# Kernel tuning notes

Hardware: AMD Instinct MI355X
Metric: run time of the kernel (lower is better)

## Reference

```python
import jax, jax.numpy as jnp
import numpy as np

EMBED = 1024
HEADS = 16
HEAD_DIM = EMBED // HEADS
B, S = 4, 2048


def setup_inputs() -> dict:
    key = jax.random.key(0)
    ks = jax.random.split(key, 12)
    scale = 1.0 / np.sqrt(EMBED)
    inp = {
        'query': jax.random.normal(ks[0], (B, S, EMBED), jnp.float32),
        'key_in': jax.random.normal(ks[1], (B, S, EMBED), jnp.float32),
        'value': jax.random.normal(ks[2], (B, S, EMBED), jnp.float32),
        'mask': jnp.tril(jnp.ones((S, S), jnp.int32))[None, None],  # causal [1,1,S,S]
        'Wq': jax.random.normal(ks[3], (EMBED, EMBED), jnp.float32) * scale,
        'bq': jnp.zeros((EMBED,), jnp.float32),
        'Wk': jax.random.normal(ks[4], (EMBED, EMBED), jnp.float32) * scale,
        'bk': jnp.zeros((EMBED,), jnp.float32),
        'Wv': jax.random.normal(ks[5], (EMBED, EMBED), jnp.float32) * scale,
        'bv': jnp.zeros((EMBED,), jnp.float32),
        'Wo': jax.random.normal(ks[6], (EMBED, EMBED), jnp.float32) * scale,
        'bo': jnp.zeros((EMBED,), jnp.float32),
    }
    return inp


def reference(query, key_in, value, mask, Wq, bq, Wk, bk, Wv, bv, Wo, bo):
    b = query.shape[0]
    # projections (torch Linear: x @ W.T + b)
    Q = query @ Wq.T + bq
    K = key_in @ Wk.T + bk
    V = value @ Wv.T + bv
    # [B, H, S, Dh]
    Q = Q.reshape(b, -1, HEADS, HEAD_DIM).transpose(0, 2, 1, 3)
    K = K.reshape(b, -1, HEADS, HEAD_DIM).transpose(0, 2, 1, 3)
    V = V.reshape(b, -1, HEADS, HEAD_DIM).transpose(0, 2, 1, 3)
    scores = jnp.einsum('bhqd,bhkd->bhqk', Q, K) / np.sqrt(HEAD_DIM)
    scores = jnp.where(mask == 0, jnp.float32(-1e20), scores)
    probs = jax.nn.softmax(scores, axis=-1)  # dropout p=0 (eval)
    attn = jnp.einsum('bhqk,bhkd->bhqd', probs, V)
    attn = attn.transpose(0, 2, 1, 3).reshape(b, -1, EMBED)
    return attn @ Wo.T + bo
```

## Files before the change

### kernel.cpp

```cpp
#include <hip/hip_runtime.h>
#include <type_traits>

typedef unsigned short u16;
typedef __bf16 bf16x8 __attribute__((ext_vector_type(8)));
typedef float f32x4 __attribute__((ext_vector_type(4)));

#define EMBED   1024
#define HEADS   16
#define HEAD_DIM 64
#define BATCH   4
#define SEQ     2048
#define MROWS   (BATCH * SEQ)

__device__ __forceinline__ u16 f2bf(float f) {
  union { __bf16 h; u16 u; } c;
  c.h = (__bf16)f;
  return c.u;
}

__device__ __forceinline__ bf16x8 cvt8(const float* p) {
  const float4 a = *(const float4*)p;
  const float4 b = *(const float4*)(p + 4);
  bf16x8 r;
  r[0] = (__bf16)a.x; r[1] = (__bf16)a.y; r[2] = (__bf16)a.z; r[3] = (__bf16)a.w;
  r[4] = (__bf16)b.x; r[5] = (__bf16)b.y; r[6] = (__bf16)b.z; r[7] = (__bf16)b.w;
  return r;
}

__device__ __forceinline__ void gload16(const u16* g, u16* lds) {
  __builtin_amdgcn_global_load_lds(
      (const __attribute__((address_space(1))) void*)g,
      (__attribute__((address_space(3))) void*)lds, 16, 0, 0);
}

__global__ __launch_bounds__(256) void cvt_bf16(
    const float* __restrict__ src, u16* __restrict__ dst, int n8)
{
  const int i = blockIdx.x * 256 + threadIdx.x;
  if (i < n8) *(bf16x8*)(dst + (size_t)i * 8) = cvt8(src + (size_t)i * 8);
}

__global__ __launch_bounds__(256) void cvt_fused(
    const float* q,  u16* dq,
    const float* k,  u16* dk,
    const float* wq, u16* dwq,
    const float* wk, u16* dwk,
    const float* wv, u16* dwv,
    const float* wo, u16* dwo,
    int n8t, int n8w)
{
  int i = blockIdx.x * 256 + threadIdx.x;
  if (i < n8t) { *(bf16x8*)(dq + (size_t)i * 8) = cvt8(q + (size_t)i * 8); return; }
  i -= n8t;
  if (i < n8t) { *(bf16x8*)(dk + (size_t)i * 8) = cvt8(k + (size_t)i * 8); return; }
  i -= n8t;
  if (i < n8w) { *(bf16x8*)(dwq + (size_t)i * 8) = cvt8(wq + (size_t)i * 8); return; }
  i -= n8w;
  if (i < n8w) { *(bf16x8*)(dwk + (size_t)i * 8) = cvt8(wk + (size_t)i * 8); return; }
  i -= n8w;
  if (i < n8w) { *(bf16x8*)(dwv + (size_t)i * 8) = cvt8(wv + (size_t)i * 8); return; }
  i -= n8w;
  if (dwo && i < n8w) { *(bf16x8*)(dwo + (size_t)i * 8) = cvt8(wo + (size_t)i * 8); }
}

__device__ __forceinline__ void swz_block(int& m0, int& n0) {
  const int gx = 8;
  int bid = blockIdx.y * gx + blockIdx.x;
  const int cpx = (gx * 64) >> 3;
  bid = (bid & 7) * cpx + (bid >> 3);
  m0 = (bid / gx) * 128;
  n0 = (bid - (bid / gx) * gx) * 128;
}

template<typename TB, typename TC>
__global__ __launch_bounds__(256) void gemm_bt(
    const u16* __restrict__ A, const TB* __restrict__ Bw,
    const float* __restrict__ bias, TC* __restrict__ C,
    int M, int N, int K)
{
  __shared__ __align__(16) u16 As[128][32];
  __shared__ __align__(16) u16 Bs[128][32];
  const int t    = threadIdx.x;
  const int lane = t & 63;
  const int wave = t >> 6;
  const int quad = lane >> 4;
  const int lr   = lane & 15;
  int m0, n0;
  swz_block(m0, n0);
  const int wr = (wave >> 1) * 64;
  const int wc = (wave & 1) * 64;
  const int gr = lane >> 2;
  const int gc = (lane & 3) * 8;

  f32x4 acc[4][4] = {};

  for (int k0 = 0; k0 < K; k0 += 32) {
    gload16(&A[(size_t)(m0 + 16 * wave + gr) * K + k0 + gc],      &As[16 * wave][0]);
    gload16(&A[(size_t)(m0 + 64 + 16 * wave + gr) * K + k0 + gc], &As[64 + 16 * wave][0]);
    if constexpr (std::is_same<TB, u16>::value) {
      gload16(&Bw[(size_t)(n0 + 16 * wave + gr) * K + k0 + gc],      &Bs[16 * wave][0]);
      gload16(&Bw[(size_t)(n0 + 64 + 16 * wave + gr) * K + k0 + gc], &Bs[64 + 16 * wave][0]);
    } else {
      const int srr = t >> 2, src = (t & 3) * 8;
      *(bf16x8*)&Bs[srr][src]      = cvt8(&Bw[(size_t)(n0 + srr) * K + k0 + src]);
      *(bf16x8*)&Bs[64 + srr][src] = cvt8(&Bw[(size_t)(n0 + 64 + srr) * K + k0 + src]);
    }
    __syncthreads();
    bf16x8 af[4], bfr[4];
#pragma unroll
    for (int i = 0; i < 4; ++i) af[i]  = *(const bf16x8*)&As[wr + i * 16 + lr][quad * 8];
#pragma unroll
    for (int i = 0; i < 4; ++i) bfr[i] = *(const bf16x8*)&Bs[wc + i * 16 + lr][quad * 8];
#pragma unroll
    for (int mi = 0; mi < 4; ++mi)
#pragma unroll
      for (int ni = 0; ni < 4; ++ni)
        acc[mi][ni] = __builtin_amdgcn_mfma_f32_16x16x32_bf16(af[mi], bfr[ni], acc[mi][ni], 0, 0, 0);
    __syncthreads();
  }

#pragma unroll
  for (int mi = 0; mi < 4; ++mi)
#pragma unroll
    for (int ni = 0; ni < 4; ++ni) {
      const int col = n0 + wc + ni * 16 + lr;
      const float bv = bias[col];
#pragma unroll
      for (int r = 0; r < 4; ++r) {
        const int row = m0 + wr + mi * 16 + quad * 4 + r;
        const float v = acc[mi][ni][r] + bv;
        if constexpr (std::is_same<TC, u16>::value)
          C[(size_t)row * N + col] = f2bf(v);
        else
          C[(size_t)row * N + col] = v;
      }
    }
}

__global__ __launch_bounds__(256) void gemm_vt(
    const u16* __restrict__ A, const u16* __restrict__ Bw,
    const float* __restrict__ bias, u16* __restrict__ Vt,
    int M, int N, int K)
{
  __shared__ __align__(16) u16 As[128][32];
  __shared__ __align__(16) u16 Bs[128][32];
  const int t    = threadIdx.x;
  const int lane = t & 63;
  const int wave = t >> 6;
  const int quad = lane >> 4;
  const int lr   = lane & 15;
  int m0, n0;
  swz_block(m0, n0);
  const int wr = (wave >> 1) * 64;
  const int wc = (wave & 1) * 64;
  const int gr = lane >> 2;
  const int gc = (lane & 3) * 8;

  f32x4 acc[4][4] = {};

  for (int k0 = 0; k0 < K; k0 += 32) {
    gload16(&A[(size_t)(m0 + 16 * wave + gr) * K + k0 + gc],       &As[16 * wave][0]);
    gload16(&A[(size_t)(m0 + 64 + 16 * wave + gr) * K + k0 + gc],  &As[64 + 16 * wave][0]);
    gload16(&Bw[(size_t)(n0 + 16 * wave + gr) * K + k0 + gc],      &Bs[16 * wave][0]);
    gload16(&Bw[(size_t)(n0 + 64 + 16 * wave + gr) * K + k0 + gc], &Bs[64 + 16 * wave][0]);
    __syncthreads();
    bf16x8 af[4], bfr[4];
#pragma unroll
    for (int i = 0; i < 4; ++i) af[i]  = *(const bf16x8*)&As[wr + i * 16 + lr][quad * 8];
#pragma unroll
    for (int i = 0; i < 4; ++i) bfr[i] = *(const bf16x8*)&Bs[wc + i * 16 + lr][quad * 8];
#pragma unroll
    for (int mi = 0; mi < 4; ++mi)
#pragma unroll
      for (int ni = 0; ni < 4; ++ni)
        acc[mi][ni] = __builtin_amdgcn_mfma_f32_16x16x32_bf16(af[mi], bfr[ni], acc[mi][ni], 0, 0, 0);
    __syncthreads();
  }

#pragma unroll
  for (int mi = 0; mi < 4; ++mi)
#pragma unroll
    for (int ni = 0; ni < 4; ++ni) {
      const int col = n0 + wc + ni * 16 + lr;
      const int hh = col >> 6, dd = col & 63;
      const float bv = bias[col];
      const int row0 = m0 + wr + mi * 16 + quad * 4;
      const int bb = row0 >> 11, s0 = row0 & 2047;
      u16 pk[4];
#pragma unroll
      for (int r = 0; r < 4; ++r) pk[r] = f2bf(acc[mi][ni][r] + bv);
      *(ushort4*)&Vt[((size_t)((bb * 16 + hh) * 64 + dd)) * SEQ + s0] = *(ushort4*)pk;
    }
}

#define QS_OFF 0
#define PS_OFF (64 * 72)
#define KV_OFF (2 * 64 * 72)
#define TILE_SZ (64 * 64)
__global__ __launch_bounds__(256, 3) void flash5(
    const u16* __restrict__ Qbf, const u16* __restrict__ Wqb,
    const float* __restrict__ bq,
    const u16* __restrict__ Kp, const u16* __restrict__ Vt,
    u16* __restrict__ AO)
{
  __shared__ __align__(16) u16 smem[KV_OFF + 4 * TILE_SZ];
  u16 (*Qs)[72] = (u16(*)[72])(smem + QS_OFF);
  u16 (*Ps)[72] = (u16(*)[72])(smem + PS_OFF);

  const int t    = threadIdx.x;
  const int lane = t & 63;
  const int wave = t >> 6;
  const int quad = lane >> 4;
  const int lr   = lane & 15;
  const int bh = blockIdx.x;
  const int pr = blockIdx.y;
  const int b  = bh >> 4, h = bh & 15;
  const size_t rowbase = (size_t)b * SEQ;
  const int hcol = h * HEAD_DIM;
  const int wrow = wave * 16;
  const int sr = lane >> 3;
  const int sc = ((lane & 7) ^ sr) * 8;

  auto frag = [&](int off, int row, int chunk) -> bf16x8 {
    return *(const bf16x8*)(smem + off + row * 64 + ((chunk ^ (row & 7)) << 3));
  };

  int q0 = 0;

  auto stageQW = [&](int bi, int k0) {
    const int ko = KV_OFF + bi * TILE_SZ;
    const int vo = KV_OFF + (2 + bi) * TILE_SZ;
#pragma unroll
    for (int c8 = 0; c8 < 2; ++c8) {
      const int g = wrow + c8 * 8;
      gload16(&Qbf[(rowbase + q0 + g + sr) * EMBED + k0 + sc], smem + ko + g * 64);
      gload16(&Wqb[(size_t)(hcol + g + sr) * EMBED + k0 + sc], smem + vo + g * 64);
    }
  };
  auto stageKV = [&](int bi, int j) {
    const int kb = j * 64;
    const int ko = KV_OFF + bi * TILE_SZ;
    const int vo = KV_OFF + (2 + bi) * TILE_SZ;
#pragma unroll
    for (int c8 = 0; c8 < 2; ++c8) {
      const int g = wrow + c8 * 8;
      gload16(&Kp[(rowbase + kb + g + sr) * EMBED + hcol + sc], smem + ko + g * 64);
      gload16(&Vt[((size_t)bh * 64 + g + sr) * SEQ + kb + sc],  smem + vo + g * 64);
    }
  };

  for (int half = 0; half < 2; ++half) {
    const int qi = half ? (31 - pr) : pr;
    q0 = qi * 64;

    f32x4 qacc[4] = {};
    stageQW(0, 0);
    __syncthreads();
    for (int s = 0; s < 16; ++s) {
      if (s < 15) stageQW((s + 1) & 1, (s + 1) * 64);
      const int ao = KV_OFF + (s & 1) * TILE_SZ;
      const int bo = KV_OFF + (2 + (s & 1)) * TILE_SZ;
#pragma unroll
      for (int ks = 0; ks < 2; ++ks) {
        const bf16x8 aq = frag(ao, wrow + lr, ks * 4 + quad);
        bf16x8 bw[4];
#pragma unroll
        for (int mi = 0; mi < 4; ++mi) bw[mi] = frag(bo, mi * 16 + lr, ks * 4 + quad);
        __builtin_amdgcn_s_setprio(1);
#pragma unroll
        for (int mi = 0; mi < 4; ++mi)
          qacc[mi] = __builtin_amdgcn_mfma_f32_16x16x32_bf16(bw[mi], aq, qacc[mi], 0, 0, 0);
        __builtin_amdgcn_s_setprio(0);
      }
      __syncthreads();
    }
#pragma unroll
    for (int mi = 0; mi < 4; ++mi) {
      const float4 bv4 = *(const float4*)&bq[hcol + mi * 16 + quad * 4];
      union { ushort4 v; u16 e[4]; } pk;
      pk.e[0] = f2bf(qacc[mi][0] + bv4.x);
      pk.e[1] = f2bf(qacc[mi][1] + bv4.y);
      pk.e[2] = f2bf(qacc[mi][2] + bv4.z);
      pk.e[3] = f2bf(qacc[mi][3] + bv4.w);
      *(ushort4*)&Qs[wrow + lr][mi * 16 + quad * 4] = pk.v;
    }

    f32x4 o_acc[4] = {};
    float lsum = 0.f;

    stageKV(0, 0);
    __syncthreads();
    for (int j = 0; j <= qi; ++j) {
      if (j < qi) stageKV((j + 1) & 1, j + 1);
      const int ko = KV_OFF + (j & 1) * TILE_SZ;
      const int vo = KV_OFF + (2 + (j & 1)) * TILE_SZ;

      f32x4 st[4] = {};
#pragma unroll
      for (int ks = 0; ks < 2; ++ks) {
        const bf16x8 a = *(const bf16x8*)&Qs[wrow + lr][ks * 32 + quad * 8];
        bf16x8 bk[4];
#pragma unroll
        for (int mi = 0; mi < 4; ++mi) bk[mi] = frag(ko, mi * 16 + lr, ks * 4 + quad);
        __builtin_amdgcn_s_setprio(1);
#pragma unroll
        for (int mi = 0; mi < 4; ++mi)
          st[mi] = __builtin_amdgcn_mfma_f32_16x16x32_bf16(bk[mi], a, st[mi], 0, 0, 0);
        __builtin_amdgcn_s_setprio(0);
      }
      const bool diag = (j == qi);
#pragma unroll
      for (int mi = 0; mi < 4; ++mi) {
        union { ushort4 v; u16 e[4]; } pk;
#pragma unroll
        for (int r = 0; r < 4; ++r) {
          float p = __expf(st[mi][r] * 0.125f);
          if (diag && (mi * 16 + quad * 4 + r > wrow + lr)) p = 0.f;
          lsum += p;
          pk.e[r] = f2bf(p);
        }
        *(ushort4*)&Ps[wrow + lr][mi * 16 + quad * 4] = pk.v;
      }
#pragma unroll
      for (int ks = 0; ks < 2; ++ks) {
        const bf16x8 ap = *(const bf16x8*)&Ps[wrow + lr][ks * 32 + quad * 8];
        bf16x8 bv[4];
#pragma unroll
        for (int nd = 0; nd < 4; ++nd) bv[nd] = frag(vo, nd * 16 + lr, ks * 4 + quad);
        __builtin_amdgcn_s_setprio(1);
#pragma unroll
        for (int nd = 0; nd < 4; ++nd)
          o_acc[nd] = __builtin_amdgcn_mfma_f32_16x16x32_bf16(ap, bv[nd], o_acc[nd], 0, 0, 0);
        __builtin_amdgcn_s_setprio(0);
      }
      __syncthreads();
    }

    lsum += __shfl_xor(lsum, 16);
    lsum += __shfl_xor(lsum, 32);
    float linv[4];
#pragma unroll
    for (int r = 0; r < 4; ++r)
      linv[r] = 1.0f / __shfl(lsum, quad * 4 + r);
#pragma unroll
    for (int nd = 0; nd < 4; ++nd)
#pragma unroll
      for (int r = 0; r < 4; ++r)
        AO[(rowbase + q0 + wrow + quad * 4 + r) * EMBED + hcol + nd * 16 + lr]
            = f2bf(o_acc[nd][r] * linv[r]);
  }
}

extern "C" void kernel_launch(void* const* d_in, const int* in_sizes, int n_in,
                              void* d_out, int out_size, void* d_ws, size_t ws_size,
                              hipStream_t stream) {
  const float* query  = (const float*)d_in[0];
  const float* key_in = (const float*)d_in[1];
  const float* value  = (const float*)d_in[2];
  const float* Wq = (const float*)d_in[4];
  const float* bq = (const float*)d_in[5];
  const float* Wk = (const float*)d_in[6];
  const float* bk = (const float*)d_in[7];
  const float* Wv = (const float*)d_in[8];
  const float* bv = (const float*)d_in[9];
  const float* Wo = (const float*)d_in[10];
  const float* bo = (const float*)d_in[11];
  float* out = (float*)d_out;

  const size_t tsz = (size_t)MROWS * EMBED;
  const size_t wsz = (size_t)EMBED * EMBED;

  u16* Kp = (u16*)d_ws;
  u16* Vt = Kp + tsz;
  const bool wo_bf = (ws_size >= (2 * tsz + wsz) * sizeof(u16));
  u16* Wob = wo_bf ? (Vt + tsz) : nullptr;

  u16* Qbf = (u16*)d_out;
  u16* Wqb = Qbf + tsz;
  u16* Wkb = Wqb + wsz;
  u16* Wvb = Wkb + wsz;

  u16* Kbf = (u16*)d_in[3];
  u16* Vbf = Kbf;
  u16* AO  = Kbf;

  dim3 blk(256);
  const int n8t = (int)(tsz / 8), n8w = (int)(wsz / 8);

  {
    const int total = 2 * n8t + (wo_bf ? 4 : 3) * n8w;
    cvt_fused<<<(total + 255) / 256, blk, 0, stream>>>(
        query, Qbf, key_in, Kbf, Wq, Wqb, Wk, Wkb, Wv, Wvb, Wo, Wob, n8t, n8w);
  }

  dim3 gproj(EMBED / 128, MROWS / 128);
  gemm_bt<u16, u16><<<gproj, blk, 0, stream>>>(Kbf, Wkb, bk, Kp, MROWS, EMBED, EMBED);

  cvt_bf16<<<n8t / 256, blk, 0, stream>>>(value, Vbf, n8t);
  gemm_vt<<<gproj, blk, 0, stream>>>(Vbf, Wvb, bv, Vt, MROWS, EMBED, EMBED);

  dim3 gattn(BATCH * HEADS, 16);
  flash5<<<gattn, blk, 0, stream>>>(Qbf, Wqb, bq, Kp, Vt, AO);

  if (wo_bf)
    gemm_bt<u16, float><<<gproj, blk, 0, stream>>>(AO, Wob, bo, out, MROWS, EMBED, EMBED);
  else
    gemm_bt<float, float><<<gproj, blk, 0, stream>>>(AO, Wo, bo, out, MROWS, EMBED, EMBED);
}
```

Measured before the change: 365.9 us.

## Fuse fp32 conversion into a batched QKV projection GEMM and simplify attention

Replaces the separate fp32-to-bf16 activation conversion kernels and the separate K and V projection GEMMs with one batched qkv_gemm launch (grid z over Q/K/V). That kernel converts fp32 inputs to bf16 while staging them into LDS. The Q projection moves out of the attention kernel, so flash6 just loads a precomputed Q tile instead of recomputing Q from Wq in every block. This removes extra activation round-trips through memory and several kernel launches. In exchange, the A operand is now loaded synchronously through registers rather than with direct-to-LDS loads, and the Q projection buffer is placed in the output buffer.

```diff
diff --git a/kernel.cpp b/kernel.cpp
--- a/kernel.cpp
+++ b/kernel.cpp
@@ -33,27 +33,12 @@
       (__attribute__((address_space(3))) void*)lds, 16, 0, 0);
 }
 
-__global__ __launch_bounds__(256) void cvt_bf16(
-    const float* __restrict__ src, u16* __restrict__ dst, int n8)
-{
-  const int i = blockIdx.x * 256 + threadIdx.x;
-  if (i < n8) *(bf16x8*)(dst + (size_t)i * 8) = cvt8(src + (size_t)i * 8);
-}
-
-__global__ __launch_bounds__(256) void cvt_fused(
-    const float* q,  u16* dq,
-    const float* k,  u16* dk,
-    const float* wq, u16* dwq,
-    const float* wk, u16* dwk,
-    const float* wv, u16* dwv,
-    const float* wo, u16* dwo,
-    int n8t, int n8w)
+__global__ __launch_bounds__(256) void cvt_w(
+    const float* wq, u16* dwq, const float* wk, u16* dwk,
+    const float* wv, u16* dwv, const float* wo, u16* dwo,
+    int n8w)
 {
   int i = blockIdx.x * 256 + threadIdx.x;
-  if (i < n8t) { *(bf16x8*)(dq + (size_t)i * 8) = cvt8(q + (size_t)i * 8); return; }
-  i -= n8t;
-  if (i < n8t) { *(bf16x8*)(dk + (size_t)i * 8) = cvt8(k + (size_t)i * 8); return; }
-  i -= n8t;
   if (i < n8w) { *(bf16x8*)(dwq + (size_t)i * 8) = cvt8(wq + (size_t)i * 8); return; }
   i -= n8w;
   if (i < n8w) { *(bf16x8*)(dwk + (size_t)i * 8) = cvt8(wk + (size_t)i * 8); return; }
@@ -70,6 +55,86 @@
   bid = (bid & 7) * cpx + (bid >> 3);
   m0 = (bid / gx) * 128;
   n0 = (bid - (bid / gx) * gx) * 128;
+}
+
+__global__ __launch_bounds__(256) void qkv_gemm(
+    const float* __restrict__ Aq, const float* __restrict__ Ak, const float* __restrict__ Av,
+    const u16* __restrict__ Wqb, const u16* __restrict__ Wkb, const u16* __restrict__ Wvb,
+    const float* __restrict__ bq, const float* __restrict__ bk, const float* __restrict__ bv,
+    u16* __restrict__ Qp, u16* __restrict__ Kp, u16* __restrict__ Vt)
+{
+  __shared__ __align__(16) u16 As[128][32];
+  __shared__ __align__(16) u16 Bs[128][32];
+  const int z = blockIdx.z;
+  const float* A    = (z == 0) ? Ak  : (z == 1) ? Av  : Aq;
+  const u16*   Bw   = (z == 0) ? Wkb : (z == 1) ? Wvb : Wqb;
+  const float* bias = (z == 0) ? bk  : (z == 1) ? bv  : bq;
+  const int K = EMBED, N = EMBED;
+
+  const int t    = threadIdx.x;
+  const int lane = t & 63;
+  const int wave = t >> 6;
+  const int quad = lane >> 4;
+  const int lr   = lane & 15;
+  int m0, n0;
+  swz_block(m0, n0);
+  const int wr = (wave >> 1) * 64;
+  const int wc = (wave & 1) * 64;
+  const int gr = lane >> 2;
+  const int gc = (lane & 3) * 8;
+  const int srr = t >> 2, src = (t & 3) * 8;
+
+  f32x4 acc[4][4] = {};
+
+  for (int k0 = 0; k0 < K; k0 += 32) {
+    *(bf16x8*)&As[srr][src]      = cvt8(&A[(size_t)(m0 + srr) * K + k0 + src]);
+    *(bf16x8*)&As[64 + srr][src] = cvt8(&A[(size_t)(m0 + 64 + srr) * K + k0 + src]);
+    gload16(&Bw[(size_t)(n0 + 16 * wave + gr) * K + k0 + gc],      &Bs[16 * wave][0]);
+    gload16(&Bw[(size_t)(n0 + 64 + 16 * wave + gr) * K + k0 + gc], &Bs[64 + 16 * wave][0]);
+    __syncthreads();
+    bf16x8 af[4], bfr[4];
+#pragma unroll
+    for (int i = 0; i < 4; ++i) af[i]  = *(const bf16x8*)&As[wr + i * 16 + lr][quad * 8];
+#pragma unroll
+    for (int i = 0; i < 4; ++i) bfr[i] = *(const bf16x8*)&Bs[wc + i * 16 + lr][quad * 8];
+#pragma unroll
+    for (int mi = 0; mi < 4; ++mi)
+#pragma unroll
+      for (int ni = 0; ni < 4; ++ni)
+        acc[mi][ni] = __builtin_amdgcn_mfma_f32_16x16x32_bf16(af[mi], bfr[ni], acc[mi][ni], 0, 0, 0);
+    __syncthreads();
+  }
+
+  if (z == 1) {
+#pragma unroll
+    for (int mi = 0; mi < 4; ++mi)
+#pragma unroll
+      for (int ni = 0; ni < 4; ++ni) {
+        const int col = n0 + wc + ni * 16 + lr;
+        const int hh = col >> 6, dd = col & 63;
+        const float bv = bias[col];
+        const int row0 = m0 + wr + mi * 16 + quad * 4;
+        const int bb = row0 >> 11, s0 = row0 & 2047;
+        u16 pk[4];
+#pragma unroll
+        for (int r = 0; r < 4; ++r) pk[r] = f2bf(acc[mi][ni][r] + bv);
+        *(ushort4*)&Vt[((size_t)((bb * 16 + hh) * 64 + dd)) * SEQ + s0] = *(ushort4*)pk;
+      }
+  } else {
+    u16* C = (z == 0) ? Kp : Qp;
+#pragma unroll
+    for (int mi = 0; mi < 4; ++mi)
+#pragma unroll
+      for (int ni = 0; ni < 4; ++ni) {
+        const int col = n0 + wc + ni * 16 + lr;
+        const float bv = bias[col];
+#pragma unroll
+        for (int r = 0; r < 4; ++r) {
+          const int row = m0 + wr + mi * 16 + quad * 4 + r;
+          C[(size_t)row * N + col] = f2bf(acc[mi][ni][r] + bv);
+        }
+      }
+  }
 }
 
 template<typename TB, typename TC>
@@ -137,74 +202,15 @@
     }
 }
 
-__global__ __launch_bounds__(256) void gemm_vt(
-    const u16* __restrict__ A, const u16* __restrict__ Bw,
-    const float* __restrict__ bias, u16* __restrict__ Vt,
-    int M, int N, int K)
-{
-  __shared__ __align__(16) u16 As[128][32];
-  __shared__ __align__(16) u16 Bs[128][32];
-  const int t    = threadIdx.x;
-  const int lane = t & 63;
-  const int wave = t >> 6;
-  const int quad = lane >> 4;
-  const int lr   = lane & 15;
-  int m0, n0;
-  swz_block(m0, n0);
-  const int wr = (wave >> 1) * 64;
-  const int wc = (wave & 1) * 64;
-  const int gr = lane >> 2;
-  const int gc = (lane & 3) * 8;
-
-  f32x4 acc[4][4] = {};
-
-  for (int k0 = 0; k0 < K; k0 += 32) {
-    gload16(&A[(size_t)(m0 + 16 * wave + gr) * K + k0 + gc],       &As[16 * wave][0]);
-    gload16(&A[(size_t)(m0 + 64 + 16 * wave + gr) * K + k0 + gc],  &As[64 + 16 * wave][0]);
-    gload16(&Bw[(size_t)(n0 + 16 * wave + gr) * K + k0 + gc],      &Bs[16 * wave][0]);
-    gload16(&Bw[(size_t)(n0 + 64 + 16 * wave + gr) * K + k0 + gc], &Bs[64 + 16 * wave][0]);
-    __syncthreads();
-    bf16x8 af[4], bfr[4];
-#pragma unroll
-    for (int i = 0; i < 4; ++i) af[i]  = *(const bf16x8*)&As[wr + i * 16 + lr][quad * 8];
-#pragma unroll
-    for (int i = 0; i < 4; ++i) bfr[i] = *(const bf16x8*)&Bs[wc + i * 16 + lr][quad * 8];
-#pragma unroll
-    for (int mi = 0; mi < 4; ++mi)
-#pragma unroll
-      for (int ni = 0; ni < 4; ++ni)
-        acc[mi][ni] = __builtin_amdgcn_mfma_f32_16x16x32_bf16(af[mi], bfr[ni], acc[mi][ni], 0, 0, 0);
-    __syncthreads();
-  }
-
-#pragma unroll
-  for (int mi = 0; mi < 4; ++mi)
-#pragma unroll
-    for (int ni = 0; ni < 4; ++ni) {
-      const int col = n0 + wc + ni * 16 + lr;
-      const int hh = col >> 6, dd = col & 63;
-      const float bv = bias[col];
-      const int row0 = m0 + wr + mi * 16 + quad * 4;
-      const int bb = row0 >> 11, s0 = row0 & 2047;
-      u16 pk[4];
-#pragma unroll
-      for (int r = 0; r < 4; ++r) pk[r] = f2bf(acc[mi][ni][r] + bv);
-      *(ushort4*)&Vt[((size_t)((bb * 16 + hh) * 64 + dd)) * SEQ + s0] = *(ushort4*)pk;
-    }
-}
-
-#define QS_OFF 0
-#define PS_OFF (64 * 72)
-#define KV_OFF (2 * 64 * 72)
+#define PS_OFF 0
+#define QT_OFF (64 * 72)
+#define KV_OFF (QT_OFF + 64 * 64)
 #define TILE_SZ (64 * 64)
-__global__ __launch_bounds__(256, 3) void flash5(
-    const u16* __restrict__ Qbf, const u16* __restrict__ Wqb,
-    const float* __restrict__ bq,
-    const u16* __restrict__ Kp, const u16* __restrict__ Vt,
-    u16* __restrict__ AO)
+__global__ __launch_bounds__(256, 3) void flash6(
+    const u16* __restrict__ Qp, const u16* __restrict__ Kp,
+    const u16* __restrict__ Vt, u16* __restrict__ AO)
 {
   __shared__ __align__(16) u16 smem[KV_OFF + 4 * TILE_SZ];
-  u16 (*Qs)[72] = (u16(*)[72])(smem + QS_OFF);
   u16 (*Ps)[72] = (u16(*)[72])(smem + PS_OFF);
 
   const int t    = threadIdx.x;
@@ -227,14 +233,11 @@
 
   int q0 = 0;
 
-  auto stageQW = [&](int bi, int k0) {
-    const int ko = KV_OFF + bi * TILE_SZ;
-    const int vo = KV_OFF + (2 + bi) * TILE_SZ;
+  auto stageQ = [&]() {
 #pragma unroll
     for (int c8 = 0; c8 < 2; ++c8) {
       const int g = wrow + c8 * 8;
-      gload16(&Qbf[(rowbase + q0 + g + sr) * EMBED + k0 + sc], smem + ko + g * 64);
-      gload16(&Wqb[(size_t)(hcol + g + sr) * EMBED + k0 + sc], smem + vo + g * 64);
+      gload16(&Qp[(rowbase + q0 + g + sr) * EMBED + hcol + sc], smem + QT_OFF + g * 64);
     }
   };
   auto stageKV = [&](int bi, int j) {
@@ -253,43 +256,13 @@
     const int qi = half ? (31 - pr) : pr;
     q0 = qi * 64;
 
-    f32x4 qacc[4] = {};
-    stageQW(0, 0);
-    __syncthreads();
-    for (int s = 0; s < 16; ++s) {
-      if (s < 15) stageQW((s + 1) & 1, (s + 1) * 64);
-      const int ao = KV_OFF + (s & 1) * TILE_SZ;
-      const int bo = KV_OFF + (2 + (s & 1)) * TILE_SZ;
-#pragma unroll
-      for (int ks = 0; ks < 2; ++ks) {
-        const bf16x8 aq = frag(ao, wrow + lr, ks * 4 + quad);
-        bf16x8 bw[4];
-#pragma unroll
-        for (int mi = 0; mi < 4; ++mi) bw[mi] = frag(bo, mi * 16 + lr, ks * 4 + quad);
-        __builtin_amdgcn_s_setprio(1);
-#pragma unroll
-        for (int mi = 0; mi < 4; ++mi)
-          qacc[mi] = __builtin_amdgcn_mfma_f32_16x16x32_bf16(bw[mi], aq, qacc[mi], 0, 0, 0);
-        __builtin_amdgcn_s_setprio(0);
-      }
-      __syncthreads();
-    }
-#pragma unroll
-    for (int mi = 0; mi < 4; ++mi) {
-      const float4 bv4 = *(const float4*)&bq[hcol + mi * 16 + quad * 4];
-      union { ushort4 v; u16 e[4]; } pk;
-      pk.e[0] = f2bf(qacc[mi][0] + bv4.x);
-      pk.e[1] = f2bf(qacc[mi][1] + bv4.y);
-      pk.e[2] = f2bf(qacc[mi][2] + bv4.z);
-      pk.e[3] = f2bf(qacc[mi][3] + bv4.w);
-      *(ushort4*)&Qs[wrow + lr][mi * 16 + quad * 4] = pk.v;
-    }
+    stageQ();
+    stageKV(0, 0);
+    __syncthreads();
 
     f32x4 o_acc[4] = {};
     float lsum = 0.f;
 
-    stageKV(0, 0);
-    __syncthreads();
     for (int j = 0; j <= qi; ++j) {
       if (j < qi) stageKV((j + 1) & 1, j + 1);
       const int ko = KV_OFF + (j & 1) * TILE_SZ;
@@ -298,7 +271,7 @@
       f32x4 st[4] = {};
 #pragma unroll
       for (int ks = 0; ks < 2; ++ks) {
-        const bf16x8 a = *(const bf16x8*)&Qs[wrow + lr][ks * 32 + quad * 8];
+        const bf16x8 a = frag(QT_OFF, wrow + lr, ks * 4 + quad);
         bf16x8 bk[4];
 #pragma unroll
         for (int mi = 0; mi < 4; ++mi) bk[mi] = frag(ko, mi * 16 + lr, ks * 4 + quad);
@@ -375,33 +348,26 @@
   const bool wo_bf = (ws_size >= (2 * tsz + wsz) * sizeof(u16));
   u16* Wob = wo_bf ? (Vt + tsz) : nullptr;
 
-  u16* Qbf = (u16*)d_out;
-  u16* Wqb = Qbf + tsz;
+  u16* Wqb = (u16*)d_out;
   u16* Wkb = Wqb + wsz;
   u16* Wvb = Wkb + wsz;
-
-  u16* Kbf = (u16*)d_in[3];
-  u16* Vbf = Kbf;
-  u16* AO  = Kbf;
+  u16* Qp  = Wvb + wsz;
+
+  u16* AO = (u16*)d_in[3];
 
   dim3 blk(256);
-  const int n8t = (int)(tsz / 8), n8w = (int)(wsz / 8);
-
-  {
-    const int total = 2 * n8t + (wo_bf ? 4 : 3) * n8w;
-    cvt_fused<<<(total + 255) / 256, blk, 0, stream>>>(
-        query, Qbf, key_in, Kbf, Wq, Wqb, Wk, Wkb, Wv, Wvb, Wo, Wob, n8t, n8w);
-  }
+  const int n8w = (int)(wsz / 8);
+
+  cvt_w<<<((wo_bf ? 4 : 3) * n8w + 255) / 256, blk, 0, stream>>>(
+      Wq, Wqb, Wk, Wkb, Wv, Wvb, Wo, Wob, n8w);
+
+  qkv_gemm<<<dim3(8, 64, 3), blk, 0, stream>>>(
+      query, key_in, value, Wqb, Wkb, Wvb, bq, bk, bv, Qp, Kp, Vt);
+
+  dim3 gattn(BATCH * HEADS, 16);
+  flash6<<<gattn, blk, 0, stream>>>(Qp, Kp, Vt, AO);
 
   dim3 gproj(EMBED / 128, MROWS / 128);
-  gemm_bt<u16, u16><<<gproj, blk, 0, stream>>>(Kbf, Wkb, bk, Kp, MROWS, EMBED, EMBED);
-
-  cvt_bf16<<<n8t / 256, blk, 0, stream>>>(value, Vbf, n8t);
-  gemm_vt<<<gproj, blk, 0, stream>>>(Vbf, Wvb, bv, Vt, MROWS, EMBED, EMBED);
-
-  dim3 gattn(BATCH * HEADS, 16);
-  flash5<<<gattn, blk, 0, stream>>>(Qbf, Wqb, bq, Kp, Vt, AO);
-
   if (wo_bf)
     gemm_bt<u16, float><<<gproj, blk, 0, stream>>>(AO, Wob, bo, out, MROWS, EMBED, EMBED);
   else
```

New measurement: 341.5 us. -6.7%, faster.
